# Kernel optimization log

Measured on AMD Instinct MI355X. Metric: run time of the kernel, lower is better.

## Reference

```python
import jax, jax.numpy as jnp
import numpy as np

OVERSAMP = 2


def _pad_last2(x, H2, W2):
    # centered zero-pad of last two dims to (H2, W2) -- PadLast
    H, W = x.shape[-2], x.shape[-1]
    ph, pw = (H2 - H) // 2, (W2 - W) // 2
    pad = [(0, 0)] * (x.ndim - 2) + [(ph, H2 - H - ph), (pw, W2 - W - pw)]
    return jnp.pad(x, pad)


def _crop_last2(x, H, W):
    # centered crop of last two dims to (H, W) -- PadLast.adjoint
    H2, W2 = x.shape[-2], x.shape[-1]
    ph, pw = (H2 - H) // 2, (W2 - W) // 2
    return x[..., ph:ph + H, pw:pw + W]


def setup_inputs() -> dict:
    key = jax.random.key(0)
    ks = jax.random.split(key, 6)
    A, C, H, W = 5, 12, 256, 256
    Hp, Wp = OVERSAMP * H, OVERSAMP * W
    x_r = jax.random.normal(ks[0], (A, H, W), dtype=jnp.float32)
    x_i = jax.random.normal(ks[1], (A, H, W), dtype=jnp.float32)
    mps_r = jax.random.normal(ks[2], (C, H, W), dtype=jnp.float32) * 0.1
    mps_i = jax.random.normal(ks[3], (C, H, W), dtype=jnp.float32) * 0.1
    kern_r = jax.random.normal(ks[4], (A, A, Hp, Wp), dtype=jnp.float32) * 0.1
    kern_i = jax.random.normal(ks[5], (A, A, Hp, Wp), dtype=jnp.float32) * 0.1
    return {"x_r": x_r, "x_i": x_i, "mps_r": mps_r, "mps_i": mps_i,
            "kern_r": kern_r, "kern_i": kern_i}


def reference(x_r, x_i, mps_r, mps_i, kern_r, kern_i):
    # Toeplitz normal operator AHA_func: x [A,H,W] -> [A,H,W]
    x = jax.lax.complex(x_r, x_i)          # [A,H,W]
    mps = jax.lax.complex(mps_r, mps_i)    # [C,H,W]
    kernels = jax.lax.complex(kern_r, kern_i)  # [Aout,Ain,2H,2W]
    A, H, W = x.shape
    Hp, Wp = kernels.shape[-2], kernels.shape[-1]
    # coil modulation: x[None,:] * mps[:,None] -> [C,A,H,W]
    cx = mps[:, None, :, :] * x[None, :, :, :]
    cx = _pad_last2(cx, Hp, Wp)            # [C,A,2H,2W]
    Fx = jnp.fft.fftn(cx, axes=(-2, -1), norm='ortho')
    # Fx[:,None] [C,1,Ain,2H,2W] * kernels [Aout,Ain,2H,2W] -> [C,Aout,Ain,2H,2W]
    y = (OVERSAMP ** 2) * jnp.fft.ifftn(Fx[:, None, ...] * kernels,
                                        axes=(-2, -1), norm='ortho')
    y = jnp.sum(y, axis=2)                 # sum over Ain -> [C,Aout,2H,2W]
    y = _crop_last2(y, H, W)               # [C,A,H,W]
    y = y * jnp.conj(mps)[:, None, :, :]
    return jnp.sum(y, axis=0)              # [A,H,W]
```

## Files before the change

### kernel.cpp

```cpp
#include <hip/hip_runtime.h>
#include <cstddef>

#define PI_F 3.14159265358979323846f
#define A_  5
#define C_  12
#define RPG (C_ * A_)

__device__ float2 g_bufA[RPG * 256 * 512];
__device__ float2 g_bufB[RPG * 512 * 256];
__device__ float2 g_kernT[25 * 512 * 512];

#define NP 528
__device__ inline int PADI(int i) { return i + (i >> 5); }

__device__ inline void build_tab256(float2* tab, int t) {
    #pragma unroll
    for (int q = 0; q < 2; ++q) {
        int k = t + q * 128;
        float s, c;
        __sincosf(-2.0f * PI_F * (float)k * (1.0f / 512.0f), &s, &c);
        tab[k] = make_float2(c, s);
    }
}

template<int DIR>
__device__ inline float2 cmulw(float2 v, float2 w) {
    float cv = w.x, sv = (DIR < 0) ? w.y : -w.y;
    return make_float2(v.x * cv - v.y * sv, v.x * sv + v.y * cv);
}

template<int DIR>
__device__ void fft512_r4(float*& sre, float*& sim, float* dre, float* dim,
                          const float2* tab, int t) {
    float *srcR = sre, *srcI = sim, *dstR = dre, *dstI = dim;
    int Ns = 1;
    #pragma unroll
    for (int s = 0; s < 4; ++s) {
        __syncthreads();
        int j = t;
        int m = j & (Ns - 1);
        int e1 = m << (7 - 2 * s);
        float2 w1 = tab[e1], w2 = tab[2 * e1];
        float2 w3 = make_float2(w1.x * w2.x - w1.y * w2.y,
                                w1.x * w2.y + w1.y * w2.x);
        int i0 = PADI(j), i1 = PADI(j + 128), i2 = PADI(j + 256), i3 = PADI(j + 384);
        float2 v0 = make_float2(srcR[i0], srcI[i0]);
        float2 v1 = cmulw<DIR>(make_float2(srcR[i1], srcI[i1]), w1);
        float2 v2 = cmulw<DIR>(make_float2(srcR[i2], srcI[i2]), w2);
        float2 v3 = cmulw<DIR>(make_float2(srcR[i3], srcI[i3]), w3);
        float2 t0 = make_float2(v0.x + v2.x, v0.y + v2.y);
        float2 t1 = make_float2(v0.x - v2.x, v0.y - v2.y);
        float2 t2 = make_float2(v1.x + v3.x, v1.y + v3.y);
        float2 t3 = make_float2(v1.x - v3.x, v1.y - v3.y);
        float2 y0 = make_float2(t0.x + t2.x, t0.y + t2.y);
        float2 y2 = make_float2(t0.x - t2.x, t0.y - t2.y);
        float2 y1, y3;
        if (DIR < 0) {
            y1 = make_float2(t1.x + t3.y, t1.y - t3.x);
            y3 = make_float2(t1.x - t3.y, t1.y + t3.x);
        } else {
            y1 = make_float2(t1.x - t3.y, t1.y + t3.x);
            y3 = make_float2(t1.x + t3.y, t1.y - t3.x);
        }
        int idxD = ((j & ~(Ns - 1)) << 2) | m;
        int o0 = PADI(idxD), o1 = PADI(idxD + Ns);
        int o2 = PADI(idxD + 2 * Ns), o3 = PADI(idxD + 3 * Ns);
        dstR[o0] = y0.x; dstI[o0] = y0.y;
        dstR[o1] = y1.x; dstI[o1] = y1.y;
        dstR[o2] = y2.x; dstI[o2] = y2.y;
        dstR[o3] = y3.x; dstI[o3] = y3.y;
        float* tr = srcR; srcR = dstR; dstR = tr;
        float* ti = srcI; srcI = dstI; dstI = ti;
        Ns <<= 2;
    }
    __syncthreads();
    #pragma unroll
    for (int q = 0; q < 2; ++q) {
        int j = t + q * 128;
        float2 w = tab[j];
        int i0 = PADI(j), i1 = PADI(j + 256);
        float2 v0 = make_float2(srcR[i0], srcI[i0]);
        float2 tw = cmulw<DIR>(make_float2(srcR[i1], srcI[i1]), w);
        dstR[i0] = v0.x + tw.x; dstI[i0] = v0.y + tw.y;
        dstR[i1] = v0.x - tw.x; dstI[i1] = v0.y - tw.y;
    }
    __syncthreads();
    sre = dstR; sim = dstI;
}

__global__ void k_kernT2(const float* __restrict__ kr, const float* __restrict__ ki,
                         float scale) {
    __shared__ float tR[32][33], tI[32][33];
    int m = blockIdx.z;
    size_t base = (size_t)m << 18;
    int c0 = blockIdx.x * 32;
    int r0 = blockIdx.y * 32;
    int tx = threadIdx.x, ty = threadIdx.y;
    for (int i = ty; i < 32; i += 8) {
        size_t idx = base + (size_t)(c0 + i) * 512 + (r0 + tx);
        tR[i][tx] = kr[idx] * scale;
        tI[i][tx] = ki[idx] * scale;
    }
    __syncthreads();
    for (int i = ty; i < 32; i += 8)
        g_kernT[base + (size_t)(r0 + i) * 512 + (c0 + tx)] =
            make_float2(tR[tx][i], tI[tx][i]);
}

__global__ void k_fft1c(const float* __restrict__ xr, const float* __restrict__ xi,
                        const float* __restrict__ mr, const float* __restrict__ mi) {
    int row = blockIdx.x;
    int ca = row >> 8;
    int ym = row & 255;
    int coil = ca / A_;
    int a = ca - coil * A_;
    int t = threadIdx.x;
    __shared__ float reA[NP], imA[NP], reB[NP], imB[NP];
    __shared__ float2 tab[256];
    build_tab256(tab, t);
    size_t xBase = ((size_t)a * 256 + ym) * 256;
    size_t mBase = ((size_t)coil * 256 + ym) * 256;
    #pragma unroll
    for (int q = 0; q < 4; ++q) {
        int x5 = t + q * 128;
        float vr = 0.f, vi = 0.f;
        if (x5 >= 128 && x5 < 384) {
            int xm = x5 - 128;
            float ar = xr[xBase + xm], ai = xi[xBase + xm];
            float br = mr[mBase + xm], bi = mi[mBase + xm];
            vr = ar * br - ai * bi;
            vi = ar * bi + ai * br;
        }
        int p = PADI(x5);
        reA[p] = vr; imA[p] = vi;
    }
    float *sre = reA, *sim = imA;
    fft512_r4<-1>(sre, sim, reB, imB, tab, t);
    float2* o = g_bufA + (size_t)row * 512;
    #pragma unroll
    for (int q = 0; q < 4; ++q) {
        int k = t + q * 128;
        int p = PADI(k);
        o[k] = make_float2(sre[p], sim[p]);
    }
}

__global__ void k_transA() {
    __shared__ float tR[32][33], tI[32][33];
    int ca = blockIdx.z;
    const float2* sIn = g_bufA + (size_t)ca * (256 * 512);
    float2* sOut = g_bufB + (size_t)ca * (512 * 256);
    int kx0 = blockIdx.x * 32, ym0 = blockIdx.y * 32;
    int tx = threadIdx.x, ty = threadIdx.y;
    for (int i = ty; i < 32; i += 8) {
        float2 v = sIn[(size_t)(ym0 + i) * 512 + kx0 + tx];
        tR[i][tx] = v.x; tI[i][tx] = v.y;
    }
    __syncthreads();
    for (int i = ty; i < 32; i += 8)
        sOut[(size_t)(kx0 + i) * 256 + ym0 + tx] =
            make_float2(tR[tx][i], tI[tx][i]);
}

__global__ void __launch_bounds__(128) k_colfmc() {
    int b = blockIdx.x;
    int j = b >> 3;
    int kx   = (b & 7) + ((j / C_) << 3);
    int coil = j % C_;
    int t = threadIdx.x;
    __shared__ float reA[NP], imA[NP], reB[NP], imB[NP];
    __shared__ float FR[A_][512], FI[A_][512];
    __shared__ float2 tab[256];
    build_tab256(tab, t);

    for (int ain = 0; ain < A_; ++ain) {
        const float4* g4 = (const float4*)(g_bufB +
            ((size_t)(coil * A_ + ain) * 512 + kx) * 256);
        float4 v = g4[t];
        int y0 = 128 + 2 * t;
        int p0 = PADI(y0), p1 = PADI(y0 + 1);
        reA[p0] = v.x; imA[p0] = v.y;
        reA[p1] = v.z; imA[p1] = v.w;
        int q0 = PADI(t), q1 = PADI(t + 384);
        reA[q0] = 0.f; imA[q0] = 0.f;
        reA[q1] = 0.f; imA[q1] = 0.f;
        float *sre = reA, *sim = imA;
        fft512_r4<-1>(sre, sim, reB, imB, tab, t);
        #pragma unroll
        for (int q = 0; q < 4; ++q) {
            int k = t + q * 128;
            int p = PADI(k);
            FR[ain][k] = sre[p];
            FI[ain][k] = sim[p];
        }
    }
    __syncthreads();

    size_t kBase = (size_t)kx << 9;
    #pragma unroll
    for (int q = 0; q < 4; ++q) {
        int ky = t + q * 128;
        float fr[A_], fi[A_];
        #pragma unroll
        for (int ain = 0; ain < A_; ++ain) {
            fr[ain] = FR[ain][ky];
            fi[ain] = FI[ain][ky];
        }
        #pragma unroll
        for (int aout = 0; aout < A_; ++aout) {
            float gr = 0.f, gi = 0.f;
            #pragma unroll
            for (int ain = 0; ain < A_; ++ain) {
                float2 k = g_kernT[((size_t)(aout * A_ + ain) << 18) + kBase + ky];
                gr += k.x * fr[ain] - k.y * fi[ain];
                gi += k.x * fi[ain] + k.y * fr[ain];
            }
            FR[aout][ky] = gr; FI[aout][ky] = gi;
        }
    }

    for (int aout = 0; aout < A_; ++aout) {
        #pragma unroll
        for (int q = 0; q < 4; ++q) {
            int k = t + q * 128;
            int p = PADI(k);
            reA[p] = FR[aout][k];
            imA[p] = FI[aout][k];
        }
        float *sre = reA, *sim = imA;
        fft512_r4<1>(sre, sim, reB, imB, tab, t);
        float4* o4 = (float4*)(g_bufB +
            ((size_t)(coil * A_ + aout) * 512 + kx) * 256);
        int y0 = 128 + 2 * t;
        int p0 = PADI(y0), p1 = PADI(y0 + 1);
        o4[t] = make_float4(sre[p0], sim[p0], sre[p1], sim[p1]);
    }
}

__global__ void k_transB() {
    __shared__ float tR[32][33], tI[32][33];
    int ca = blockIdx.z;
    const float2* sIn = g_bufB + (size_t)ca * (512 * 256);
    float2* sOut = g_bufA + (size_t)ca * (256 * 512);
    int ym0 = blockIdx.x * 32, kx0 = blockIdx.y * 32;
    int tx = threadIdx.x, ty = threadIdx.y;
    for (int i = ty; i < 32; i += 8) {
        float2 v = sIn[(size_t)(kx0 + i) * 256 + ym0 + tx];
        tR[i][tx] = v.x; tI[i][tx] = v.y;
    }
    __syncthreads();
    for (int i = ty; i < 32; i += 8)
        sOut[(size_t)(ym0 + i) * 512 + kx0 + tx] =
            make_float2(tR[tx][i], tI[tx][i]);
}

__global__ void k_outifft() {
    int row = blockIdx.x;
    int t = threadIdx.x;
    __shared__ float reA[NP], imA[NP], reB[NP], imB[NP];
    __shared__ float2 tab[256];
    build_tab256(tab, t);
    const float4* s4 = (const float4*)(g_bufA + (size_t)row * 512);
    #pragma unroll
    for (int q = 0; q < 2; ++q) {
        int e = t + q * 128;
        float4 v = s4[e];
        int p0 = PADI(2 * e), p1 = PADI(2 * e + 1);
        reA[p0] = v.x; imA[p0] = v.y;
        reA[p1] = v.z; imA[p1] = v.w;
    }
    float *sre = reA, *sim = imA;
    fft512_r4<1>(sre, sim, reB, imB, tab, t);
    float4* o4 = (float4*)(g_bufB + (size_t)row * 256);
    int w0 = 128 + 2 * t;
    int p0 = PADI(w0), p1 = PADI(w0 + 1);
    o4[t] = make_float4(sre[p0], sim[p0], sre[p1], sim[p1]);
}

__global__ void k_outred(const float* __restrict__ mr, const float* __restrict__ mi,
                         float* __restrict__ out, int outFloats) {
    int row = blockIdx.x;
    int a = row >> 8;
    int h = row & 255;
    int w = threadIdx.x;
    float ar = 0.f, ai = 0.f;
    #pragma unroll
    for (int c = 0; c < C_; ++c) {
        float2 v = g_bufB[(((size_t)(c * A_ + a) * 256 + h)) * 256 + w];
        size_t mIdx = ((size_t)c * 256 + h) * 256 + w;
        float br = mr[mIdx], bi = -mi[mIdx];
        ar += v.x * br - v.y * bi;
        ai += v.x * bi + v.y * br;
    }
    size_t p = ((size_t)a * 256 + h) * 256 + w;
    size_t reIdx = p, imIdx = 327680 + p;
    if (reIdx < (size_t)outFloats) out[reIdx] = ar;
    if (imIdx < (size_t)outFloats) out[imIdx] = ai;
}

extern "C" void kernel_launch(void* const* d_in, const int* in_sizes, int n_in,
                              void* d_out, int out_size, void* d_ws, size_t ws_size,
                              hipStream_t stream) {
    const float* xr = (const float*)d_in[0];
    const float* xi = (const float*)d_in[1];
    const float* mr = (const float*)d_in[2];
    const float* mi = (const float*)d_in[3];
    const float* kr = (const float*)d_in[4];
    const float* ki = (const float*)d_in[5];
    float* out = (float*)d_out;
    (void)d_ws; (void)ws_size; (void)n_in; (void)in_sizes;

    const float scale = 4.0f / 262144.0f;

    k_kernT2 <<<dim3(16, 16, 25), dim3(32, 8), 0, stream>>>(kr, ki, scale);
    k_fft1c  <<<RPG * 256, 128, 0, stream>>>(xr, xi, mr, mi);
    k_transA <<<dim3(16, 8, RPG), dim3(32, 8), 0, stream>>>();
    k_colfmc <<<C_ * 512, 128, 0, stream>>>();
    k_transB <<<dim3(8, 16, RPG), dim3(32, 8), 0, stream>>>();
    k_outifft<<<RPG * 256, 128, 0, stream>>>();
    k_outred <<<A_ * 256, 256, 0, stream>>>(mr, mi, out, out_size);
}
```

Measured before the change: 332.5 us.

## Restructure pipeline: transpose inputs, drop intermediate transposes, fuse coil reduction

Transposes the small x and coil-map inputs up front so the first FFT runs along the other axis. The separate transpose kernels between FFT passes are dropped: the column kernel reads strided columns directly from the row-FFT buffer. The kernel-matrix transpose is also dropped, and raw kernel values are read per ky row with the scale applied inline. The final inverse FFT is fused with the conjugate coil-map multiply and coil reduction, followed by a small output transpose. This removes several full passes over large intermediate buffers, at the cost of strided global gathers in the column and output kernels and higher register use from the 25-element kernel arrays.

```diff
diff --git a/kernel.cpp b/kernel.cpp
--- a/kernel.cpp
+++ b/kernel.cpp
@@ -8,18 +8,21 @@
 
 __device__ float2 g_bufA[RPG * 256 * 512];
 __device__ float2 g_bufB[RPG * 512 * 256];
-__device__ float2 g_kernT[25 * 512 * 512];
+__device__ float2 g_xT[5  * 65536];
+__device__ float2 g_mT[12 * 65536];
+__device__ float2 g_oT[5  * 65536];
 
 #define NP 528
 __device__ inline int PADI(int i) { return i + (i >> 5); }
-
-__device__ inline void build_tab256(float2* tab, int t) {
+__device__ inline int PADT(int i) { return i + (i >> 3); }
+
+__device__ inline void build_tabP(float2* tab, int t) {
     #pragma unroll
     for (int q = 0; q < 2; ++q) {
         int k = t + q * 128;
         float s, c;
         __sincosf(-2.0f * PI_F * (float)k * (1.0f / 512.0f), &s, &c);
-        tab[k] = make_float2(c, s);
+        tab[PADT(k)] = make_float2(c, s);
     }
 }
 
@@ -30,9 +33,9 @@
 }
 
 template<int DIR>
-__device__ void fft512_r4(float*& sre, float*& sim, float* dre, float* dim,
-                          const float2* tab, int t) {
-    float *srcR = sre, *srcI = sim, *dstR = dre, *dstI = dim;
+__device__ void fft512(float* Ar, float* Ai, float* Br, float* Bi,
+                       const float2* tab, int t) {
+    float *srcR = Ar, *srcI = Ai, *dstR = Br, *dstI = Bi;
     int Ns = 1;
     #pragma unroll
     for (int s = 0; s < 4; ++s) {
@@ -40,7 +43,7 @@
         int j = t;
         int m = j & (Ns - 1);
         int e1 = m << (7 - 2 * s);
-        float2 w1 = tab[e1], w2 = tab[2 * e1];
+        float2 w1 = tab[PADT(e1)], w2 = tab[PADT(2 * e1)];
         float2 w3 = make_float2(w1.x * w2.x - w1.y * w2.y,
                                 w1.x * w2.y + w1.y * w2.x);
         int i0 = PADI(j), i1 = PADI(j + 128), i2 = PADI(j + 256), i3 = PADI(j + 384);
@@ -77,7 +80,7 @@
     #pragma unroll
     for (int q = 0; q < 2; ++q) {
         int j = t + q * 128;
-        float2 w = tab[j];
+        float2 w = tab[PADT(j)];
         int i0 = PADI(j), i1 = PADI(j + 256);
         float2 v0 = make_float2(srcR[i0], srcI[i0]);
         float2 tw = cmulw<DIR>(make_float2(srcR[i1], srcI[i1]), w);
@@ -85,217 +88,195 @@
         dstR[i1] = v0.x - tw.x; dstI[i1] = v0.y - tw.y;
     }
     __syncthreads();
-    sre = dstR; sim = dstI;
-}
-
-__global__ void k_kernT2(const float* __restrict__ kr, const float* __restrict__ ki,
-                         float scale) {
+}
+
+__global__ void k_inT(const float* __restrict__ xr, const float* __restrict__ xi,
+                      const float* __restrict__ mr, const float* __restrict__ mi) {
     __shared__ float tR[32][33], tI[32][33];
-    int m = blockIdx.z;
-    size_t base = (size_t)m << 18;
-    int c0 = blockIdx.x * 32;
-    int r0 = blockIdx.y * 32;
+    int z = blockIdx.z;
+    const float* pr; const float* pi; float2* dst;
+    if (z < 5) {
+        pr = xr + (size_t)z * 65536; pi = xi + (size_t)z * 65536;
+        dst = g_xT + (size_t)z * 65536;
+    } else {
+        int c = z - 5;
+        pr = mr + (size_t)c * 65536; pi = mi + (size_t)c * 65536;
+        dst = g_mT + (size_t)c * 65536;
+    }
+    int w0 = blockIdx.x * 32, h0 = blockIdx.y * 32;
     int tx = threadIdx.x, ty = threadIdx.y;
     for (int i = ty; i < 32; i += 8) {
-        size_t idx = base + (size_t)(c0 + i) * 512 + (r0 + tx);
-        tR[i][tx] = kr[idx] * scale;
-        tI[i][tx] = ki[idx] * scale;
+        size_t idx = (size_t)(h0 + i) * 256 + (w0 + tx);
+        tR[i][tx] = pr[idx];
+        tI[i][tx] = pi[idx];
     }
     __syncthreads();
     for (int i = ty; i < 32; i += 8)
-        g_kernT[base + (size_t)(r0 + i) * 512 + (c0 + tx)] =
+        dst[(size_t)(w0 + i) * 256 + (h0 + tx)] =
             make_float2(tR[tx][i], tI[tx][i]);
 }
 
-__global__ void k_fft1c(const float* __restrict__ xr, const float* __restrict__ xi,
-                        const float* __restrict__ mr, const float* __restrict__ mi) {
+__global__ void k_fft1c() {
     int row = blockIdx.x;
     int ca = row >> 8;
-    int ym = row & 255;
+    int xcol = row & 255;
     int coil = ca / A_;
     int a = ca - coil * A_;
     int t = threadIdx.x;
-    __shared__ float reA[NP], imA[NP], reB[NP], imB[NP];
-    __shared__ float2 tab[256];
-    build_tab256(tab, t);
-    size_t xBase = ((size_t)a * 256 + ym) * 256;
-    size_t mBase = ((size_t)coil * 256 + ym) * 256;
-    #pragma unroll
-    for (int q = 0; q < 4; ++q) {
-        int x5 = t + q * 128;
-        float vr = 0.f, vi = 0.f;
-        if (x5 >= 128 && x5 < 384) {
-            int xm = x5 - 128;
-            float ar = xr[xBase + xm], ai = xi[xBase + xm];
-            float br = mr[mBase + xm], bi = mi[mBase + xm];
-            vr = ar * br - ai * bi;
-            vi = ar * bi + ai * br;
-        }
-        int p = PADI(x5);
-        reA[p] = vr; imA[p] = vi;
-    }
-    float *sre = reA, *sim = imA;
-    fft512_r4<-1>(sre, sim, reB, imB, tab, t);
-    float2* o = g_bufA + (size_t)row * 512;
+    __shared__ float Are[NP], Aim[NP], Bre[NP], Bim[NP];
+    __shared__ float2 tab[288];
+    build_tabP(tab, t);
+    const float2* xs = g_xT + (size_t)a * 65536 + (size_t)xcol * 256;
+    const float2* ms = g_mT + (size_t)coil * 65536 + (size_t)xcol * 256;
+    Are[PADI(t)] = 0.f;       Aim[PADI(t)] = 0.f;
+    Are[PADI(t + 384)] = 0.f; Aim[PADI(t + 384)] = 0.f;
+    {
+        float2 xv = xs[t], mv = ms[t];
+        int p = PADI(t + 128);
+        Are[p] = xv.x * mv.x - xv.y * mv.y;
+        Aim[p] = xv.x * mv.y + xv.y * mv.x;
+        xv = xs[t + 128]; mv = ms[t + 128];
+        p = PADI(t + 256);
+        Are[p] = xv.x * mv.x - xv.y * mv.y;
+        Aim[p] = xv.x * mv.y + xv.y * mv.x;
+    }
+    fft512<-1>(Are, Aim, Bre, Bim, tab, t);
+    float2* o = (float2*)g_bufA + (size_t)row * 512;
     #pragma unroll
     for (int q = 0; q < 4; ++q) {
         int k = t + q * 128;
         int p = PADI(k);
-        o[k] = make_float2(sre[p], sim[p]);
-    }
-}
-
-__global__ void k_transA() {
-    __shared__ float tR[32][33], tI[32][33];
-    int ca = blockIdx.z;
-    const float2* sIn = g_bufA + (size_t)ca * (256 * 512);
-    float2* sOut = g_bufB + (size_t)ca * (512 * 256);
-    int kx0 = blockIdx.x * 32, ym0 = blockIdx.y * 32;
-    int tx = threadIdx.x, ty = threadIdx.y;
-    for (int i = ty; i < 32; i += 8) {
-        float2 v = sIn[(size_t)(ym0 + i) * 512 + kx0 + tx];
-        tR[i][tx] = v.x; tI[i][tx] = v.y;
-    }
-    __syncthreads();
-    for (int i = ty; i < 32; i += 8)
-        sOut[(size_t)(kx0 + i) * 256 + ym0 + tx] =
-            make_float2(tR[tx][i], tI[tx][i]);
-}
-
-__global__ void __launch_bounds__(128) k_colfmc() {
+        o[k] = make_float2(Bre[p], Bim[p]);
+    }
+}
+
+__global__ void __launch_bounds__(128) k_colfmc(const float* __restrict__ kr,
+                                                const float* __restrict__ ki) {
     int b = blockIdx.x;
-    int j = b >> 3;
-    int kx   = (b & 7) + ((j / C_) << 3);
-    int coil = j % C_;
+    int xcd = b & 7;
+    int s = b >> 3;
+    int v = s / 96, w = s % 96;
+    int u = xcd + (v << 3);
+    int coil = w % C_;
+    int ky = (u << 3) + (w / C_);
     int t = threadIdx.x;
-    __shared__ float reA[NP], imA[NP], reB[NP], imB[NP];
-    __shared__ float FR[A_][512], FI[A_][512];
-    __shared__ float2 tab[256];
-    build_tab256(tab, t);
+    __shared__ float Sre[NP], Sim[NP];
+    __shared__ float FR[A_][NP], FI[A_][NP];
+    __shared__ float2 tab[288];
+    build_tabP(tab, t);
 
     for (int ain = 0; ain < A_; ++ain) {
-        const float4* g4 = (const float4*)(g_bufB +
-            ((size_t)(coil * A_ + ain) * 512 + kx) * 256);
-        float4 v = g4[t];
-        int y0 = 128 + 2 * t;
-        int p0 = PADI(y0), p1 = PADI(y0 + 1);
-        reA[p0] = v.x; imA[p0] = v.y;
-        reA[p1] = v.z; imA[p1] = v.w;
-        int q0 = PADI(t), q1 = PADI(t + 384);
-        reA[q0] = 0.f; imA[q0] = 0.f;
-        reA[q1] = 0.f; imA[q1] = 0.f;
-        float *sre = reA, *sim = imA;
-        fft512_r4<-1>(sre, sim, reB, imB, tab, t);
-        #pragma unroll
-        for (int q = 0; q < 4; ++q) {
-            int k = t + q * 128;
-            int p = PADI(k);
-            FR[ain][k] = sre[p];
-            FI[ain][k] = sim[p];
-        }
-    }
-    __syncthreads();
-
-    size_t kBase = (size_t)kx << 9;
+        const float2* src = (const float2*)g_bufA +
+                            ((size_t)(coil * A_ + ain) << 17);
+        float2 v1 = src[(size_t)t * 512 + ky];
+        float2 v2 = src[(size_t)(t + 128) * 512 + ky];
+        Sre[PADI(t)] = 0.f;       Sim[PADI(t)] = 0.f;
+        Sre[PADI(t + 384)] = 0.f; Sim[PADI(t + 384)] = 0.f;
+        int p = PADI(t + 128);
+        Sre[p] = v1.x; Sim[p] = v1.y;
+        p = PADI(t + 256);
+        Sre[p] = v2.x; Sim[p] = v2.y;
+        fft512<-1>(Sre, Sim, FR[ain], FI[ain], tab, t);
+    }
+
+    const float scale = 4.0f / 262144.0f;
+    size_t kyBase = (size_t)ky << 9;
     #pragma unroll
     for (int q = 0; q < 4; ++q) {
-        int ky = t + q * 128;
+        int kx = t + q * 128;
+        float krB[25], kiB[25];
+        #pragma unroll
+        for (int m = 0; m < 25; ++m) {
+            size_t idx = ((size_t)m << 18) + kyBase + kx;
+            krB[m] = kr[idx];
+            kiB[m] = ki[idx];
+        }
+        int p = PADI(kx);
         float fr[A_], fi[A_];
         #pragma unroll
         for (int ain = 0; ain < A_; ++ain) {
-            fr[ain] = FR[ain][ky];
-            fi[ain] = FI[ain][ky];
+            fr[ain] = FR[ain][p];
+            fi[ain] = FI[ain][p];
         }
         #pragma unroll
         for (int aout = 0; aout < A_; ++aout) {
             float gr = 0.f, gi = 0.f;
             #pragma unroll
             for (int ain = 0; ain < A_; ++ain) {
-                float2 k = g_kernT[((size_t)(aout * A_ + ain) << 18) + kBase + ky];
-                gr += k.x * fr[ain] - k.y * fi[ain];
-                gi += k.x * fi[ain] + k.y * fr[ain];
+                float kre = krB[aout * A_ + ain], kim = kiB[aout * A_ + ain];
+                gr += kre * fr[ain] - kim * fi[ain];
+                gi += kre * fi[ain] + kim * fr[ain];
             }
-            FR[aout][ky] = gr; FI[aout][ky] = gi;
+            FR[aout][p] = scale * gr;
+            FI[aout][p] = scale * gi;
         }
     }
 
     for (int aout = 0; aout < A_; ++aout) {
+        fft512<1>(FR[aout], FI[aout], Sre, Sim, tab, t);
+        float4* o4 = (float4*)((float2*)g_bufB +
+            ((size_t)(coil * A_ + aout) * 512 + ky) * 256);
+        int x0 = 128 + 2 * t;
+        int p0 = PADI(x0), p1 = PADI(x0 + 1);
+        o4[t] = make_float4(Sre[p0], Sim[p0], Sre[p1], Sim[p1]);
+    }
+}
+
+__global__ void k_outfr() {
+    int b = blockIdx.x;
+    int xcd = b & 7;
+    int s = b >> 3;
+    int v = s >> 3, w = s & 7;
+    int g = xcd + (v << 3);
+    int a = g >> 5;
+    int xcol = ((g & 31) << 3) + w;
+    int t = threadIdx.x;
+    __shared__ float Are[NP], Aim[NP], Bre[NP], Bim[NP];
+    __shared__ float2 tab[288];
+    build_tabP(tab, t);
+    float ar0 = 0.f, ai0 = 0.f, ar1 = 0.f, ai1 = 0.f;
+    int y0 = 128 + 2 * t;
+    for (int c = 0; c < C_; ++c) {
+        const float2* src = (const float2*)g_bufB +
+                            ((size_t)(c * A_ + a) << 17);
         #pragma unroll
         for (int q = 0; q < 4; ++q) {
-            int k = t + q * 128;
-            int p = PADI(k);
-            reA[p] = FR[aout][k];
-            imA[p] = FI[aout][k];
-        }
-        float *sre = reA, *sim = imA;
-        fft512_r4<1>(sre, sim, reB, imB, tab, t);
-        float4* o4 = (float4*)(g_bufB +
-            ((size_t)(coil * A_ + aout) * 512 + kx) * 256);
-        int y0 = 128 + 2 * t;
+            int kyq = t + q * 128;
+            float2 vv = src[(size_t)kyq * 256 + xcol];
+            int p = PADI(kyq);
+            Are[p] = vv.x; Aim[p] = vv.y;
+        }
+        fft512<1>(Are, Aim, Bre, Bim, tab, t);
+        const float4* mp4 = (const float4*)(g_mT + (size_t)c * 65536 +
+                                            (size_t)xcol * 256);
+        float4 mm = mp4[t];
         int p0 = PADI(y0), p1 = PADI(y0 + 1);
-        o4[t] = make_float4(sre[p0], sim[p0], sre[p1], sim[p1]);
-    }
-}
-
-__global__ void k_transB() {
+        float v0x = Bre[p0], v0y = Bim[p0];
+        float v1x = Bre[p1], v1y = Bim[p1];
+        ar0 += v0x * mm.x + v0y * mm.y;  ai0 += v0y * mm.x - v0x * mm.y;
+        ar1 += v1x * mm.z + v1y * mm.w;  ai1 += v1y * mm.z - v1x * mm.w;
+    }
+    float4* o4 = (float4*)(g_oT + (size_t)a * 65536 + (size_t)xcol * 256);
+    o4[t] = make_float4(ar0, ai0, ar1, ai1);
+}
+
+__global__ void k_outT(float* __restrict__ out, int outFloats) {
     __shared__ float tR[32][33], tI[32][33];
-    int ca = blockIdx.z;
-    const float2* sIn = g_bufB + (size_t)ca * (512 * 256);
-    float2* sOut = g_bufA + (size_t)ca * (256 * 512);
-    int ym0 = blockIdx.x * 32, kx0 = blockIdx.y * 32;
+    int a = blockIdx.z;
+    int x0 = blockIdx.x * 32, y0 = blockIdx.y * 32;
+    const float2* src = g_oT + (size_t)a * 65536;
     int tx = threadIdx.x, ty = threadIdx.y;
     for (int i = ty; i < 32; i += 8) {
-        float2 v = sIn[(size_t)(kx0 + i) * 256 + ym0 + tx];
-        tR[i][tx] = v.x; tI[i][tx] = v.y;
-    }
-    __syncthreads();
-    for (int i = ty; i < 32; i += 8)
-        sOut[(size_t)(ym0 + i) * 512 + kx0 + tx] =
-            make_float2(tR[tx][i], tI[tx][i]);
-}
-
-__global__ void k_outifft() {
-    int row = blockIdx.x;
-    int t = threadIdx.x;
-    __shared__ float reA[NP], imA[NP], reB[NP], imB[NP];
-    __shared__ float2 tab[256];
-    build_tab256(tab, t);
-    const float4* s4 = (const float4*)(g_bufA + (size_t)row * 512);
-    #pragma unroll
-    for (int q = 0; q < 2; ++q) {
-        int e = t + q * 128;
-        float4 v = s4[e];
-        int p0 = PADI(2 * e), p1 = PADI(2 * e + 1);
-        reA[p0] = v.x; imA[p0] = v.y;
-        reA[p1] = v.z; imA[p1] = v.w;
-    }
-    float *sre = reA, *sim = imA;
-    fft512_r4<1>(sre, sim, reB, imB, tab, t);
-    float4* o4 = (float4*)(g_bufB + (size_t)row * 256);
-    int w0 = 128 + 2 * t;
-    int p0 = PADI(w0), p1 = PADI(w0 + 1);
-    o4[t] = make_float4(sre[p0], sim[p0], sre[p1], sim[p1]);
-}
-
-__global__ void k_outred(const float* __restrict__ mr, const float* __restrict__ mi,
-                         float* __restrict__ out, int outFloats) {
-    int row = blockIdx.x;
-    int a = row >> 8;
-    int h = row & 255;
-    int w = threadIdx.x;
-    float ar = 0.f, ai = 0.f;
-    #pragma unroll
-    for (int c = 0; c < C_; ++c) {
-        float2 v = g_bufB[(((size_t)(c * A_ + a) * 256 + h)) * 256 + w];
-        size_t mIdx = ((size_t)c * 256 + h) * 256 + w;
-        float br = mr[mIdx], bi = -mi[mIdx];
-        ar += v.x * br - v.y * bi;
-        ai += v.x * bi + v.y * br;
-    }
-    size_t p = ((size_t)a * 256 + h) * 256 + w;
-    size_t reIdx = p, imIdx = 327680 + p;
-    if (reIdx < (size_t)outFloats) out[reIdx] = ar;
-    if (imIdx < (size_t)outFloats) out[imIdx] = ai;
+        float2 vv = src[(size_t)(x0 + i) * 256 + (y0 + tx)];
+        tR[i][tx] = vv.x; tI[i][tx] = vv.y;
+    }
+    __syncthreads();
+    for (int i = ty; i < 32; i += 8) {
+        size_t reIdx = (size_t)a * 65536 + (size_t)(y0 + i) * 256 + (x0 + tx);
+        size_t imIdx = 327680 + reIdx;
+        if (reIdx < (size_t)outFloats) out[reIdx] = tR[tx][i];
+        if (imIdx < (size_t)outFloats) out[imIdx] = tI[tx][i];
+    }
 }
 
 extern "C" void kernel_launch(void* const* d_in, const int* in_sizes, int n_in,
@@ -310,13 +291,9 @@
     float* out = (float*)d_out;
     (void)d_ws; (void)ws_size; (void)n_in; (void)in_sizes;
 
-    const float scale = 4.0f / 262144.0f;
-
-    k_kernT2 <<<dim3(16, 16, 25), dim3(32, 8), 0, stream>>>(kr, ki, scale);
-    k_fft1c  <<<RPG * 256, 128, 0, stream>>>(xr, xi, mr, mi);
-    k_transA <<<dim3(16, 8, RPG), dim3(32, 8), 0, stream>>>();
-    k_colfmc <<<C_ * 512, 128, 0, stream>>>();
-    k_transB <<<dim3(8, 16, RPG), dim3(32, 8), 0, stream>>>();
-    k_outifft<<<RPG * 256, 128, 0, stream>>>();
-    k_outred <<<A_ * 256, 256, 0, stream>>>(mr, mi, out, out_size);
-}
+    k_inT   <<<dim3(8, 8, 17), dim3(32, 8), 0, stream>>>(xr, xi, mr, mi);
+    k_fft1c <<<RPG * 256, 128, 0, stream>>>();
+    k_colfmc<<<C_ * 512, 128, 0, stream>>>(kr, ki);
+    k_outfr <<<A_ * 256, 128, 0, stream>>>();
+    k_outT  <<<dim3(8, 8, 5), dim3(32, 8), 0, stream>>>(out, out_size);
+}
```

New measurement: 312.6 us. -6.0%, faster.
